# Kernel tuning notes

Hardware: AMD Instinct MI355X
Metric: run time of the kernel (lower is better)

Reference implementation:

```python
import jax, jax.numpy as jnp
import numpy as np

N, DX1, DX2, DH = 16384, 1024, 1024, 2048


def _linear_params(key, din, dout):
    kw, kb = jax.random.split(key)
    bound = 1.0 / np.sqrt(din)
    W = jax.random.uniform(kw, (din, dout), jnp.float32, -bound, bound)
    b = jax.random.uniform(kb, (dout,), jnp.float32, -bound, bound)
    return W, b


def setup_inputs() -> dict:
    key = jax.random.key(0)
    ks = jax.random.split(key, 8)
    X1 = jax.random.normal(ks[0], (N, DX1), jnp.float32)
    X2 = jax.random.normal(ks[1], (N, DX2), jnp.float32)
    Y = jax.random.normal(ks[2], (N, 1), jnp.float32)
    w1h_W, w1h_b = _linear_params(ks[3], DX1, DH)
    w2h_W, w2h_b = _linear_params(ks[4], DX2, DH)
    wh1_W, wh1_b = _linear_params(ks[5], DH, DX1)
    wh2_W, wh2_b = _linear_params(ks[6], DH, DX2)
    who_W, who_b = _linear_params(ks[7], DH, 1)
    return dict(X1=X1, X2=X2, Y=Y,
                w1h_W=w1h_W, w1h_b=w1h_b, w2h_W=w2h_W, w2h_b=w2h_b,
                wh1_W=wh1_W, wh1_b=wh1_b, wh2_W=wh2_W, wh2_b=wh2_b,
                who_W=who_W, who_b=who_b)


def _row_sqnorm(x):
    # algebraic rewrite of torch.diag(x @ x.T): per-row sum of squares, shape [N, 1]
    return jnp.sum(x * x, axis=1, keepdims=True)


def reference(X1, X2, Y, w1h_W, w1h_b, w2h_W, w2h_b,
              wh1_W, wh1_b, wh2_W, wh2_b, who_W, who_b):
    lin = lambda x, W, b: x @ W + b
    H1 = lin(X1, w1h_W, w1h_b)              # [N, DH]
    H2 = lin(X2, w2h_W, w2h_b)              # [N, DH]
    X2p = lin(H1, wh2_W, wh2_b)             # [N, DX2]
    X1p = lin(H2, wh1_W, wh1_b)             # [N, DX1]
    L1 = _row_sqnorm(X2p - X2)              # [N, 1]
    L2 = _row_sqnorm(X1p - X1)
    L3 = _row_sqnorm(H1 - H2)
    L4 = lin(H1 + H2, who_W, who_b) * 0.5 - Y  # [N, 1]
    # loss = sum of squares of each per-row term (Li.T @ Li)
    loss = (jnp.sum(L1 * L1) + jnp.sum(L2 * L2)
            + jnp.sum(L3 * L3) + jnp.sum(L4 * L4))
    return loss
```

## Files before the change

### kernel.cpp

```cpp
#include <hip/hip_runtime.h>
#include <cstdint>
#include <cstddef>

#define NR 16384
#define DX 1024
#define DH 2048

typedef unsigned short u16;
typedef _Float16 half8 __attribute__((ext_vector_type(8)));
typedef _Float16 half4v __attribute__((ext_vector_type(4)));
typedef float f32x4 __attribute__((ext_vector_type(4)));

__device__ __forceinline__ u16 f2h_bits(float v) {
    union { _Float16 h; u16 u; } c;
    c.h = (_Float16)v;
    return c.u;
}

__device__ __forceinline__ float h2f_bits(u16 v) {
    union { u16 u; _Float16 h; } c;
    c.u = v;
    return (float)c.h;
}

__device__ __forceinline__ void gl_lds16(const void* g, void* l) {
    __builtin_amdgcn_global_load_lds(
        (const __attribute__((address_space(1))) void*)g,
        (__attribute__((address_space(3))) void*)l, 16, 0, 0);
}

__global__ __launch_bounds__(256) void cast_f32_f16(const float* __restrict__ in,
                                                    u16* __restrict__ out) {
    size_t i = ((size_t)blockIdx.x * 256 + threadIdx.x) * 4;
    float4 v = *(const float4*)&in[i];
    half4v o = { (_Float16)v.x, (_Float16)v.y, (_Float16)v.z, (_Float16)v.w };
    *(half4v*)&out[i] = o;
}

__global__ __launch_bounds__(256) void transpose_cast(const float* __restrict__ in,
                                                      u16* __restrict__ out,
                                                      int K, int D) {
    __shared__ float tile[32][33];
    int tx = threadIdx.x & 31;
    int ty = threadIdx.x >> 5;
    int d0 = blockIdx.x * 32, k0 = blockIdx.y * 32;
#pragma unroll
    for (int i = 0; i < 32; i += 8)
        tile[ty + i][tx] = in[(size_t)(k0 + ty + i) * D + d0 + tx];
    __syncthreads();
#pragma unroll
    for (int i = 0; i < 32; i += 8)
        out[(size_t)(d0 + ty + i) * K + k0 + tx] = f2h_bits(tile[tx][ty + i]);
}

template <int MODE>
__global__ __launch_bounds__(512, 2) void gemm256(
    const u16* __restrict__ A, const u16* __restrict__ Bt,
    const float* __restrict__ bias,
    u16* __restrict__ C, const float* __restrict__ Xref,
    float* __restrict__ Lacc,
    const u16* __restrict__ Hoth, const float* __restrict__ Wo,
    float* __restrict__ L4o,
    int M, int N, int K) {
    __shared__ __align__(16) u16 As[2][16384];
    __shared__ __align__(16) u16 Bs[2][16384];

    const int nwg = gridDim.x;
    const int bid = blockIdx.x;
    const int cpx = nwg >> 3;
    const int wg  = (bid & 7) * cpx + (bid >> 3);
    const int NBN = N >> 8;
    const int m0 = (wg / NBN) * 256;
    const int n0 = (wg % NBN) * 256;

    const int tid  = threadIdx.x;
    const int lane = tid & 63;
    const int w    = tid >> 6;
    const int wr   = w >> 2;
    const int wn   = w & 3;
    const int fr   = lane & 15;
    const int qa   = (lane >> 4) * 8;
    const int NT   = K >> 6;

    f32x4 acc[8][4] = {};

    const int sx = (fr & 7) << 3;
    int aofK[2], bofK[2];
#pragma unroll
    for (int ks = 0; ks < 2; ++ks) {
        aofK[ks] = (((wr * 128 + fr) * 64) + qa + ks * 32) ^ sx;
        bofK[ks] = (((wn * 64 + fr) * 64) + qa + ks * 32) ^ sx;
    }

    const int stg_c = ((tid & 7) ^ ((tid >> 3) & 7)) << 3;
    const int stg_r = tid >> 3;
    const int stg_w = (tid >> 6) << 9;

#define STAGE(G, ldK, rowbase, kt, lbase, half_idx)                            \
    do {                                                                       \
        const u16* _s = (G) + (size_t)((rowbase) + (half_idx) * 128 + stg_r) * \
                                  (ldK) + (kt) * 64 + stg_c;                   \
        u16* _d = (lbase) + (half_idx) * 8192 + stg_w;                         \
        gl_lds16(_s, _d);                                                      \
        gl_lds16(_s + (size_t)64 * (ldK), _d + 4096);                          \
    } while (0)

#define MFMA_(d, av, bv) \
    d = __builtin_amdgcn_mfma_f32_16x16x32_f16(av, bv, d, 0, 0, 0)

    STAGE(A, K, m0, 0, &As[0][0], 0);
    STAGE(Bt, K, n0, 0, &Bs[0][0], 0);
    STAGE(A, K, m0, 0, &As[0][0], 1);
    STAGE(Bt, K, n0, 0, &Bs[0][0], 1);
    STAGE(Bt, K, n0, 1, &Bs[1][0], 0);
    STAGE(A, K, m0, 1, &As[1][0], 0);
    asm volatile("s_waitcnt vmcnt(4)" ::: "memory");
    __builtin_amdgcn_s_barrier();

    for (int t = 0; t < NT; ++t) {
        const int bb = t & 1;
        const u16* Ab = &As[bb][0];
        const u16* Bb = &Bs[bb][0];
        u16* Acur = &As[bb][0];
        u16* Bcur = &Bs[bb][0];
        u16* Anx  = &As[bb ^ 1][0];
        u16* Bnx  = &Bs[bb ^ 1][0];
        half8 af[4][2], bf[4][2];

#pragma unroll
        for (int m = 0; m < 4; ++m)
#pragma unroll
            for (int ks = 0; ks < 2; ++ks)
                af[m][ks] = *(const half8*)&Ab[aofK[ks] + m * 1024];
#pragma unroll
        for (int n = 0; n < 2; ++n)
#pragma unroll
            for (int ks = 0; ks < 2; ++ks)
                bf[n][ks] = *(const half8*)&Bb[bofK[ks] + n * 1024];
        if (t + 1 < NT) STAGE(A, K, m0, t + 1, Anx, 1);
        __builtin_amdgcn_s_barrier();
        asm volatile("s_waitcnt lgkmcnt(0)" ::: "memory");
        __builtin_amdgcn_s_setprio(1);
#pragma unroll
        for (int m = 0; m < 4; ++m)
#pragma unroll
            for (int n = 0; n < 2; ++n)
#pragma unroll
                for (int ks = 0; ks < 2; ++ks)
                    MFMA_(acc[m][n], af[m][ks], bf[n][ks]);
        __builtin_amdgcn_s_setprio(0);
        __builtin_amdgcn_s_barrier();

#pragma unroll
        for (int n = 2; n < 4; ++n)
#pragma unroll
            for (int ks = 0; ks < 2; ++ks)
                bf[n][ks] = *(const half8*)&Bb[bofK[ks] + n * 1024];
        if (t + 1 < NT) STAGE(Bt, K, n0, t + 1, Bnx, 1);
        __builtin_amdgcn_s_barrier();
        asm volatile("s_waitcnt lgkmcnt(0)" ::: "memory");
        __builtin_amdgcn_s_setprio(1);
#pragma unroll
        for (int m = 0; m < 4; ++m)
#pragma unroll
            for (int n = 2; n < 4; ++n)
#pragma unroll
                for (int ks = 0; ks < 2; ++ks)
                    MFMA_(acc[m][n], af[m][ks], bf[n][ks]);
        __builtin_amdgcn_s_setprio(0);
        __builtin_amdgcn_s_barrier();

#pragma unroll
        for (int m = 0; m < 4; ++m)
#pragma unroll
            for (int ks = 0; ks < 2; ++ks)
                af[m][ks] = *(const half8*)&Ab[aofK[ks] + 4096 + m * 1024];
        if (t + 2 < NT) STAGE(Bt, K, n0, t + 2, Bcur, 0);
        __builtin_amdgcn_s_barrier();
        asm volatile("s_waitcnt lgkmcnt(0)" ::: "memory");
        __builtin_amdgcn_s_setprio(1);
#pragma unroll
        for (int m = 0; m < 4; ++m)
#pragma unroll
            for (int n = 0; n < 2; ++n)
#pragma unroll
                for (int ks = 0; ks < 2; ++ks)
                    MFMA_(acc[4 + m][n], af[m][ks], bf[n][ks]);
        __builtin_amdgcn_s_setprio(0);
        __builtin_amdgcn_s_barrier();

        if (t + 2 < NT) STAGE(A, K, m0, t + 2, Acur, 0);
        __builtin_amdgcn_s_barrier();
        __builtin_amdgcn_s_setprio(1);
#pragma unroll
        for (int m = 0; m < 4; ++m)
#pragma unroll
            for (int n = 2; n < 4; ++n)
#pragma unroll
                for (int ks = 0; ks < 2; ++ks)
                    MFMA_(acc[4 + m][n], af[m][ks], bf[n][ks]);
        __builtin_amdgcn_s_setprio(0);
        if (t + 2 < NT)
            asm volatile("s_waitcnt vmcnt(4)" ::: "memory");
        else
            asm volatile("s_waitcnt vmcnt(0)" ::: "memory");
        __builtin_amdgcn_s_barrier();
    }

    const int colbase = n0 + wn * 64 + fr;
    float bj[4];
#pragma unroll
    for (int j = 0; j < 4; ++j) bj[j] = bias[colbase + j * 16];

    if (MODE == 0) {
#pragma unroll
        for (int i = 0; i < 8; ++i) {
            int rowb = m0 + wr * 128 + i * 16 + (lane >> 4) * 4;
#pragma unroll
            for (int r = 0; r < 4; ++r) {
                size_t ro = (size_t)(rowb + r) * N;
#pragma unroll
                for (int j = 0; j < 4; ++j)
                    C[ro + colbase + j * 16] = f2h_bits(acc[i][j][r] + bj[j]);
            }
        }
    } else if (MODE == 1) {
#pragma unroll
        for (int i = 0; i < 8; ++i) {
            int rowb = m0 + wr * 128 + i * 16 + (lane >> 4) * 4;
#pragma unroll
            for (int r = 0; r < 4; ++r) {
                size_t ro = (size_t)(rowb + r) * N;
                float s = 0.f;
#pragma unroll
                for (int j = 0; j < 4; ++j) {
                    float d = acc[i][j][r] + bj[j] - Xref[ro + colbase + j * 16];
                    s += d * d;
                }
                s += __shfl_xor(s, 1, 64);
                s += __shfl_xor(s, 2, 64);
                s += __shfl_xor(s, 4, 64);
                s += __shfl_xor(s, 8, 64);
                if (fr == 0) atomicAdd(&Lacc[rowb + r], s);
            }
        }
    } else {
        float wj[4];
#pragma unroll
        for (int j = 0; j < 4; ++j) wj[j] = Wo[colbase + j * 16];
#pragma unroll
        for (int i = 0; i < 8; ++i) {
            int rowb = m0 + wr * 128 + i * 16 + (lane >> 4) * 4;
#pragma unroll
            for (int r = 0; r < 4; ++r) {
                size_t ro = (size_t)(rowb + r) * N;
                float s3 = 0.f, s4 = 0.f;
#pragma unroll
                for (int j = 0; j < 4; ++j) {
                    float h2 = acc[i][j][r] + bj[j];
                    C[ro + colbase + j * 16] = f2h_bits(h2);
                    float h1 = h2f_bits(Hoth[ro + colbase + j * 16]);
                    float d = h1 - h2;
                    s3 += d * d;
                    s4 += (h1 + h2) * wj[j];
                }
                s3 += __shfl_xor(s3, 1, 64);
                s3 += __shfl_xor(s3, 2, 64);
                s3 += __shfl_xor(s3, 4, 64);
                s3 += __shfl_xor(s3, 8, 64);
                s4 += __shfl_xor(s4, 1, 64);
                s4 += __shfl_xor(s4, 2, 64);
                s4 += __shfl_xor(s4, 4, 64);
                s4 += __shfl_xor(s4, 8, 64);
                if (fr == 0) {
                    atomicAdd(&Lacc[rowb + r], s3);
                    atomicAdd(&L4o[rowb + r], s4);
                }
            }
        }
    }
#undef STAGE
#undef MFMA_
}

__global__ __launch_bounds__(1024) void final_reduce(
    const float* __restrict__ L1, const float* __restrict__ L2,
    const float* __restrict__ L3, const float* __restrict__ L4,
    const float* __restrict__ Y, const float* __restrict__ whob,
    float* __restrict__ out) {
    float s = 0.f;
    float wb = whob[0];
    for (int r = threadIdx.x; r < NR; r += 1024) {
        float l4 = 0.5f * (L4[r] + wb) - Y[r];
        s += L1[r] * L1[r] + L2[r] * L2[r] + L3[r] * L3[r] + l4 * l4;
    }
#pragma unroll
    for (int off = 1; off < 64; off <<= 1) s += __shfl_xor(s, off, 64);
    __shared__ float sm[16];
    int w = threadIdx.x >> 6, ln = threadIdx.x & 63;
    if (ln == 0) sm[w] = s;
    __syncthreads();
    if (threadIdx.x == 0) {
        float t = 0.f;
#pragma unroll
        for (int i = 0; i < 16; ++i) t += sm[i];
        out[0] = t;
    }
}

extern "C" void kernel_launch(void* const* d_in, const int* in_sizes, int n_in,
                              void* d_out, int out_size, void* d_ws, size_t ws_size,
                              hipStream_t stream) {
    const float* X1   = (const float*)d_in[0];
    const float* X2   = (const float*)d_in[1];
    const float* Y    = (const float*)d_in[2];
    const float* w1hW = (const float*)d_in[3];
    const float* w1hb = (const float*)d_in[4];
    const float* w2hW = (const float*)d_in[5];
    const float* w2hb = (const float*)d_in[6];
    const float* wh1W = (const float*)d_in[7];
    const float* wh1b = (const float*)d_in[8];
    const float* wh2W = (const float*)d_in[9];
    const float* wh2b = (const float*)d_in[10];
    const float* whoW = (const float*)d_in[11];
    const float* whob = (const float*)d_in[12];

    char* ws = (char*)d_ws;
    u16* X1h  = (u16*)(ws);
    u16* X2h  = X1h + (size_t)NR * DX;
    u16* H1h  = X2h + (size_t)NR * DX;
    u16* H2h  = H1h + (size_t)NR * DH;
    u16* w1hT = H2h + (size_t)NR * DH;
    u16* w2hT = w1hT + (size_t)DH * DX;
    u16* wh1T = w2hT + (size_t)DH * DX;
    u16* wh2T = wh1T + (size_t)DX * DH;
    float* L1a = (float*)(wh2T + (size_t)DX * DH);
    float* L2a = L1a + NR;
    float* L3a = L2a + NR;
    float* L4a = L3a + NR;

    hipMemsetAsync(L1a, 0, 4 * (size_t)NR * sizeof(float), stream);

    cast_f32_f16<<<NR * DX / 1024, 256, 0, stream>>>(X1, X1h);
    cast_f32_f16<<<NR * DX / 1024, 256, 0, stream>>>(X2, X2h);
    transpose_cast<<<dim3(DH / 32, DX / 32), 256, 0, stream>>>(w1hW, w1hT, DX, DH);
    transpose_cast<<<dim3(DH / 32, DX / 32), 256, 0, stream>>>(w2hW, w2hT, DX, DH);
    transpose_cast<<<dim3(DX / 32, DH / 32), 256, 0, stream>>>(wh1W, wh1T, DH, DX);
    transpose_cast<<<dim3(DX / 32, DH / 32), 256, 0, stream>>>(wh2W, wh2T, DH, DX);

    gemm256<0><<<dim3((NR / 256) * (DH / 256)), 512, 0, stream>>>(
        X1h, w1hT, w1hb, H1h, nullptr, nullptr, nullptr, nullptr, nullptr,
        NR, DH, DX);
    gemm256<2><<<dim3((NR / 256) * (DH / 256)), 512, 0, stream>>>(
        X2h, w2hT, w2hb, H2h, nullptr, L3a, H1h, whoW, L4a,
        NR, DH, DX);

    gemm256<1><<<dim3((NR / 256) * (DX / 256)), 512, 0, stream>>>(
        H1h, wh2T, wh2b, nullptr, X2, L1a, nullptr, nullptr, nullptr,
        NR, DX, DH);
    gemm256<1><<<dim3((NR / 256) * (DX / 256)), 512, 0, stream>>>(
        H2h, wh1T, wh1b, nullptr, X1, L2a, nullptr, nullptr, nullptr,
        NR, DX, DH);

    final_reduce<<<1, 1024, 0, stream>>>(L1a, L2a, L3a, L4a, Y, whob, (float*)d_out);
}
```

Measured before the change: 558.9 us.

## Stage GEMM epilogue through LDS for vectorized stores and parallelize final reduce

```diff
diff --git a/kernel.cpp b/kernel.cpp
--- a/kernel.cpp
+++ b/kernel.cpp
@@ -15,12 +15,6 @@
     union { _Float16 h; u16 u; } c;
     c.h = (_Float16)v;
     return c.u;
-}
-
-__device__ __forceinline__ float h2f_bits(u16 v) {
-    union { u16 u; _Float16 h; } c;
-    c.u = v;
-    return (float)c.h;
 }
 
 __device__ __forceinline__ void gl_lds16(const void* g, void* l) {
@@ -207,74 +201,77 @@
         __builtin_amdgcn_s_barrier();
     }
 
+    float* scratch = (float*)&As[0][0] + (size_t)w * 1088;
+    const int q  = lane >> 4;
+    const int sr = lane >> 3;
+    const int cc = (lane & 7) * 8;
+
     const int colbase = n0 + wn * 64 + fr;
     float bj[4];
 #pragma unroll
     for (int j = 0; j < 4; ++j) bj[j] = bias[colbase + j * 16];
 
-    if (MODE == 0) {
-#pragma unroll
-        for (int i = 0; i < 8; ++i) {
-            int rowb = m0 + wr * 128 + i * 16 + (lane >> 4) * 4;
-#pragma unroll
-            for (int r = 0; r < 4; ++r) {
-                size_t ro = (size_t)(rowb + r) * N;
-#pragma unroll
-                for (int j = 0; j < 4; ++j)
-                    C[ro + colbase + j * 16] = f2h_bits(acc[i][j][r] + bj[j]);
+#pragma unroll
+    for (int i = 0; i < 8; ++i) {
+#pragma unroll
+        for (int j = 0; j < 4; ++j)
+#pragma unroll
+            for (int r = 0; r < 4; ++r)
+                scratch[(q * 4 + r) * 68 + fr + j * 16] = acc[i][j][r] + bj[j];
+#pragma unroll
+        for (int h = 0; h < 2; ++h) {
+            const int r16 = h * 8 + sr;
+            const float* src = &scratch[r16 * 68 + cc];
+            float v[8];
+            *(f32x4*)&v[0] = *(const f32x4*)&src[0];
+            *(f32x4*)&v[4] = *(const f32x4*)&src[4];
+            const int rowg = m0 + wr * 128 + i * 16 + r16;
+            const int colg = n0 + wn * 64 + cc;
+            const size_t off = (size_t)rowg * N + colg;
+
+            if (MODE == 0 || MODE == 2) {
+                half8 hv;
+#pragma unroll
+                for (int u = 0; u < 8; ++u) hv[u] = (_Float16)v[u];
+                *(half8*)&C[off] = hv;
             }
-        }
-    } else if (MODE == 1) {
-#pragma unroll
-        for (int i = 0; i < 8; ++i) {
-            int rowb = m0 + wr * 128 + i * 16 + (lane >> 4) * 4;
-#pragma unroll
-            for (int r = 0; r < 4; ++r) {
-                size_t ro = (size_t)(rowb + r) * N;
+            if (MODE == 1) {
+                float4 x0 = *(const float4*)&Xref[off];
+                float4 x1 = *(const float4*)&Xref[off + 4];
+                float xr[8] = { x0.x, x0.y, x0.z, x0.w, x1.x, x1.y, x1.z, x1.w };
                 float s = 0.f;
 #pragma unroll
-                for (int j = 0; j < 4; ++j) {
-                    float d = acc[i][j][r] + bj[j] - Xref[ro + colbase + j * 16];
+                for (int u = 0; u < 8; ++u) {
+                    float d = v[u] - xr[u];
                     s += d * d;
                 }
                 s += __shfl_xor(s, 1, 64);
                 s += __shfl_xor(s, 2, 64);
                 s += __shfl_xor(s, 4, 64);
-                s += __shfl_xor(s, 8, 64);
-                if (fr == 0) atomicAdd(&Lacc[rowb + r], s);
+                if ((lane & 7) == 0) atomicAdd(&Lacc[rowg], s);
             }
-        }
-    } else {
-        float wj[4];
-#pragma unroll
-        for (int j = 0; j < 4; ++j) wj[j] = Wo[colbase + j * 16];
-#pragma unroll
-        for (int i = 0; i < 8; ++i) {
-            int rowb = m0 + wr * 128 + i * 16 + (lane >> 4) * 4;
-#pragma unroll
-            for (int r = 0; r < 4; ++r) {
-                size_t ro = (size_t)(rowb + r) * N;
+            if (MODE == 2) {
+                half8 hh = *(const half8*)&Hoth[off];
+                float4 w0 = *(const float4*)&Wo[colg];
+                float4 w1 = *(const float4*)&Wo[colg + 4];
+                float wv[8] = { w0.x, w0.y, w0.z, w0.w, w1.x, w1.y, w1.z, w1.w };
                 float s3 = 0.f, s4 = 0.f;
 #pragma unroll
-                for (int j = 0; j < 4; ++j) {
-                    float h2 = acc[i][j][r] + bj[j];
-                    C[ro + colbase + j * 16] = f2h_bits(h2);
-                    float h1 = h2f_bits(Hoth[ro + colbase + j * 16]);
-                    float d = h1 - h2;
+                for (int u = 0; u < 8; ++u) {
+                    float h1 = (float)hh[u];
+                    float d = h1 - v[u];
                     s3 += d * d;
-                    s4 += (h1 + h2) * wj[j];
+                    s4 += (h1 + v[u]) * wv[u];
                 }
                 s3 += __shfl_xor(s3, 1, 64);
                 s3 += __shfl_xor(s3, 2, 64);
                 s3 += __shfl_xor(s3, 4, 64);
-                s3 += __shfl_xor(s3, 8, 64);
                 s4 += __shfl_xor(s4, 1, 64);
                 s4 += __shfl_xor(s4, 2, 64);
                 s4 += __shfl_xor(s4, 4, 64);
-                s4 += __shfl_xor(s4, 8, 64);
-                if (fr == 0) {
-                    atomicAdd(&Lacc[rowb + r], s3);
-                    atomicAdd(&L4o[rowb + r], s4);
+                if ((lane & 7) == 0) {
+                    atomicAdd(&Lacc[rowg], s3);
+                    atomicAdd(&L4o[rowg], s4);
                 }
             }
         }
@@ -283,29 +280,23 @@
 #undef MFMA_
 }
 
-__global__ __launch_bounds__(1024) void final_reduce(
+__global__ __launch_bounds__(256) void final_reduce(
     const float* __restrict__ L1, const float* __restrict__ L2,
     const float* __restrict__ L3, const float* __restrict__ L4,
     const float* __restrict__ Y, const float* __restrict__ whob,
     float* __restrict__ out) {
-    float s = 0.f;
+    int r = blockIdx.x * 256 + threadIdx.x;
     float wb = whob[0];
-    for (int r = threadIdx.x; r < NR; r += 1024) {
-        float l4 = 0.5f * (L4[r] + wb) - Y[r];
-        s += L1[r] * L1[r] + L2[r] * L2[r] + L3[r] * L3[r] + l4 * l4;
-    }
+    float l4 = 0.5f * (L4[r] + wb) - Y[r];
+    float s = L1[r] * L1[r] + L2[r] * L2[r] + L3[r] * L3[r] + l4 * l4;
 #pragma unroll
     for (int off = 1; off < 64; off <<= 1) s += __shfl_xor(s, off, 64);
-    __shared__ float sm[16];
+    __shared__ float sm[4];
     int w = threadIdx.x >> 6, ln = threadIdx.x & 63;
     if (ln == 0) sm[w] = s;
     __syncthreads();
-    if (threadIdx.x == 0) {
-        float t = 0.f;
-#pragma unroll
-        for (int i = 0; i < 16; ++i) t += sm[i];
-        out[0] = t;
-    }
+    if (threadIdx.x == 0)
+        atomicAdd(out, sm[0] + sm[1] + sm[2] + sm[3]);
 }
 
 extern "C" void kernel_launch(void* const* d_in, const int* in_sizes, int n_in,
@@ -340,6 +331,7 @@
     float* L4a = L3a + NR;
 
     hipMemsetAsync(L1a, 0, 4 * (size_t)NR * sizeof(float), stream);
+    hipMemsetAsync(d_out, 0, sizeof(float), stream);
 
     cast_f32_f16<<<NR * DX / 1024, 256, 0, stream>>>(X1, X1h);
     cast_f32_f16<<<NR * DX / 1024, 256, 0, stream>>>(X2, X2h);
@@ -362,5 +354,6 @@
         H2h, wh1T, wh1b, nullptr, X1, L2a, nullptr, nullptr, nullptr,
         NR, DX, DH);
 
-    final_reduce<<<1, 1024, 0, stream>>>(L1a, L2a, L3a, L4a, Y, whob, (float*)d_out);
-}
+    final_reduce<<<NR / 256, 256, 0, stream>>>(L1a, L2a, L3a, L4a, Y, whob,
+                                               (float*)d_out);
+}
```

Measured after the change: 528.6 us. 5.4% less time.
